# Kernel tuning notes

Hardware: AMD Instinct MI355X
Metric: run time of the kernel (lower is better)

## Reference

```python
import jax, jax.numpy as jnp
import numpy as np

B, N, D = 8, 10000, 16
E = 320000
EH, EOUT, NOUT = 32, 30, 64

def setup_inputs() -> dict:
    key = jax.random.key(0)
    ks = jax.random.split(key, 12)
    x = jax.random.normal(ks[0], (B, N, D), dtype=jnp.float32)
    edge_index = jax.random.randint(ks[1], (2, E), 0, N, dtype=jnp.int32)
    # edge_attr: col 0 = city distance (keep away from 0), col 1 = direction
    dist = jax.random.uniform(ks[2], (E,), dtype=jnp.float32) * 100.0 + 1.0
    direc = jax.random.uniform(ks[3], (E,), dtype=jnp.float32) * 360.0
    edge_attr = jnp.stack([dist, direc], axis=-1)
    wind_mean = jnp.array([3.0, 180.0], dtype=jnp.float32)
    wind_std = jnp.array([1.5, 90.0], dtype=jnp.float32)
    W1 = jax.random.normal(ks[4], (2 * D + 2 + 1, EH), dtype=jnp.float32) * 0.1
    b1 = jnp.zeros((EH,), dtype=jnp.float32)
    W2 = jax.random.normal(ks[5], (EH, EOUT), dtype=jnp.float32) * 0.1
    b2 = jnp.zeros((EOUT,), dtype=jnp.float32)
    Wn = jax.random.normal(ks[6], (EOUT, NOUT), dtype=jnp.float32) * 0.1
    bn = jnp.zeros((NOUT,), dtype=jnp.float32)
    return {"x": x, "edge_index": edge_index, "edge_attr": edge_attr,
            "wind_mean": wind_mean, "wind_std": wind_std,
            "W1": W1, "b1": b1, "W2": W2, "b2": b2, "Wn": Wn, "bn": bn}

def reference(x, edge_index, edge_attr, wind_mean, wind_std, W1, b1, W2, b2, Wn, bn):
    src, tgt = edge_index[0], edge_index[1]
    node_src = x[:, src]      # [B, E, D]
    node_tgt = x[:, tgt]      # [B, E, D]
    # de-normalize wind features (last 2 channels)
    src_wind = node_src[:, :, -2:] * wind_std[None, None, :] + wind_mean[None, None, :]
    speed = src_wind[:, :, 0]
    direc = src_wind[:, :, 1]
    city_dist = edge_attr[:, 0][None, :]   # [1, E]
    city_direc = edge_attr[:, 1][None, :]
    theta = jnp.abs(city_direc - direc)
    edge_weight = jax.nn.relu(3.0 * speed * jnp.cos(theta) / city_dist)  # [B, E]
    # normalized edge attributes (torch std is unbiased)
    ea_norm = (edge_attr - edge_attr.mean(axis=0)) / jnp.std(edge_attr, axis=0, ddof=1)
    ea_norm_b = jnp.broadcast_to(ea_norm[None, :, :], (x.shape[0], ea_norm.shape[0], 2))
    feat = jnp.concatenate([node_src, node_tgt, ea_norm_b, edge_weight[:, :, None]], axis=-1)  # [B, E, 2D+3]
    h = jax.nn.sigmoid(feat @ W1 + b1)
    e = jax.nn.sigmoid(h @ W2 + b2)        # [B, E, EOUT]
    agg = jnp.zeros((x.shape[0], x.shape[1], e.shape[-1]), dtype=e.dtype)
    agg = agg.at[:, tgt].add(e)
    agg = agg.at[:, src].add(-e)
    out = jax.nn.sigmoid(agg @ Wn + bn)    # [B, N, NOUT]
    return out
```

## Files before the change

### kernel.cpp

```cpp
#include <hip/hip_runtime.h>
#include <hip/hip_bf16.h>
#include <math.h>

#define B 8
#define N 10000
#define D 16
#define E 320000
#define EH 32
#define EOUT 30
#define NOUT 64
#define FEAT 35
#define FILL_BLOCKS ((E + 255) / 256)
#define PQ_BLOCKS   ((B * N * 64) / 256)

typedef short bf16x8 __attribute__((ext_vector_type(8)));
typedef float f32x4 __attribute__((ext_vector_type(4)));

#define LDS_FENCE() asm volatile("" ::: "memory")

__device__ __forceinline__ float sigmoidf_(float v) {
    return __builtin_amdgcn_rcpf(1.0f + __expf(-v));
}

__device__ __forceinline__ unsigned int pack_bf16_2(float a, float b) {
    unsigned ua = __float_as_uint(a), ub = __float_as_uint(b);
    ua = (ua + 0x7FFFu + ((ua >> 16) & 1u)) >> 16;
    ub = (ub + 0x7FFFu + ((ub >> 16) & 1u)) >> 16;
    return ua | (ub << 16);
}

__device__ __forceinline__ unsigned short bf16rn(float f) {
    unsigned u = __float_as_uint(f);
    u = (u + 0x7FFFu + ((u >> 16) & 1u)) >> 16;
    return (unsigned short)u;
}

__global__ void stats_count_kernel(const float* __restrict__ ea,
                                   const int* __restrict__ eidx,
                                   float* __restrict__ stats,
                                   int* __restrict__ cnt) {
    float s0 = 0.f, s1 = 0.f, q0 = 0.f, q1 = 0.f;
    for (int i = blockIdx.x * blockDim.x + threadIdx.x; i < E; i += gridDim.x * blockDim.x) {
        float2 v = *(const float2*)(ea + 2 * (size_t)i);
        s0 += v.x; q0 += v.x * v.x;
        s1 += v.y; q1 += v.y * v.y;
        atomicAdd(&cnt[eidx[E + i]], 1);
        atomicAdd(&cnt[N + eidx[i]], 1);
    }
    #pragma unroll
    for (int off = 32; off > 0; off >>= 1) {
        s0 += __shfl_down(s0, off);
        s1 += __shfl_down(s1, off);
        q0 += __shfl_down(q0, off);
        q1 += __shfl_down(q1, off);
    }
    if ((threadIdx.x & 63) == 0) {
        atomicAdd(&stats[0], s0);
        atomicAdd(&stats[1], s1);
        atomicAdd(&stats[2], q0);
        atomicAdd(&stats[3], q1);
    }
}

__global__ void __launch_bounds__(1024) scan_kernel(const int* __restrict__ cnt_in,
                                                    int* __restrict__ offs,
                                                    int* __restrict__ cursor,
                                                    float* __restrict__ stats,
                                                    const float* __restrict__ W2,
                                                    unsigned short* __restrict__ w2f) {
    if (threadIdx.x == 0) {
        const float n = (float)E;
        float s0 = stats[0], s1 = stats[1], q0 = stats[2], q1 = stats[3];
        float v0 = (q0 - s0 * s0 / n) / (n - 1.0f);
        float v1 = (q1 - s1 * s1 / n) / (n - 1.0f);
        stats[4] = s0 / n;
        stats[5] = 1.0f / sqrtf(v0);
        stats[6] = s1 / n;
        stats[7] = 1.0f / sqrtf(v1);
    }
    if (threadIdx.x < 128) {
        int tl = threadIdx.x >> 6;
        int ln = threadIdx.x & 63;
        int k0 = (ln >> 4) * 8;
        int col = tl * 16 + (ln & 15);
        unsigned short* hi = w2f + ((size_t)(tl * 2 + 0) * 64 + ln) * 8;
        unsigned short* lo = w2f + ((size_t)(tl * 2 + 1) * 64 + ln) * 8;
        #pragma unroll
        for (int j = 0; j < 8; j++) {
            float w = (col < EOUT) ? W2[(k0 + j) * EOUT + col] : 0.0f;
            unsigned u = __float_as_uint(w) & 0xFFFF0000u;
            float r = w - __uint_as_float(u);
            hi[j] = (unsigned short)(u >> 16);
            lo[j] = bf16rn(r);
        }
    }
    const int M = 2 * N;
    const int CH = 20;
    __shared__ int lds[1024];
    int t = threadIdx.x;
    int base = t * CH;
    int loc[CH];
    int s = 0;
    #pragma unroll
    for (int i = 0; i < CH; i++) {
        int idx = base + i;
        int v = (idx < M) ? cnt_in[idx] : 0;
        loc[i] = s;
        s += v;
    }
    lds[t] = s;
    __syncthreads();
    for (int off = 1; off < 1024; off <<= 1) {
        int v = (t >= off) ? lds[t - off] : 0;
        __syncthreads();
        lds[t] += v;
        __syncthreads();
    }
    int tbase = (t > 0) ? lds[t - 1] : 0;
    #pragma unroll
    for (int i = 0; i < CH; i++) {
        int idx = base + i;
        if (idx < M) {
            offs[idx] = tbase + loc[i];
            cursor[idx] = tbase + loc[i];
        }
    }
    if (t == 1023) offs[M] = lds[1023];
}

__global__ void __launch_bounds__(256) fill_pq_kernel(
    const int* __restrict__ eidx, int* __restrict__ cursor,
    int* __restrict__ lists,
    const float* __restrict__ x, const float* __restrict__ W1,
    const float* __restrict__ b1,
    unsigned short* __restrict__ Pb, unsigned short* __restrict__ Qb)
{
    if (blockIdx.x < FILL_BLOCKS) {
        int e = blockIdx.x * 256 + threadIdx.x;
        if (e >= E) return;
        int p = atomicAdd(&cursor[eidx[E + e]], 1);
        lists[p] = e;
        int q = atomicAdd(&cursor[N + eidx[e]], 1);
        lists[q] = e;
    } else {
        int wid = ((blockIdx.x - FILL_BLOCKS) * 256 + threadIdx.x) >> 6;
        int lane = threadIdx.x & 63;
        if (wid >= B * N) return;
        int j = lane & 31;
        int half = lane >> 5;
        const float* xr = x + (size_t)wid * D;
        float acc = half ? b1[j] : 0.f;
        const float* Wb = W1 + (half ? D * EH : 0);
        #pragma unroll
        for (int d = 0; d < D; d++)
            acc = fmaf(xr[d], Wb[d * EH + j], acc);
        float accN = __shfl_down(acc, 1);
        if (!(lane & 1)) {
            unsigned u = pack_bf16_2(acc, accN);
            unsigned short* dst = (half ? Qb : Pb) + (size_t)wid * EH + j;
            *(unsigned*)dst = u;
        }
    }
}

__global__ void __launch_bounds__(256) edge_mlp_kernel(
    const float* __restrict__ x, const int* __restrict__ eidx,
    const float* __restrict__ ea,
    const float* __restrict__ wind_mean, const float* __restrict__ wind_std,
    const float* __restrict__ W1, const float* __restrict__ b2,
    const float* __restrict__ stats,
    const unsigned short* __restrict__ Pb, const unsigned short* __restrict__ Qb,
    const unsigned short* __restrict__ w2f,
    unsigned short* __restrict__ eBuf, int b0, int nb)
{
    __shared__ unsigned short hsh[4][64][64];

    int t = blockIdx.x * blockDim.x + threadIdx.x;
    if (t >= nb * E) return;
    int bb = t / E;
    int e = t - bb * E;
    int b = b0 + bb;
    int wv = threadIdx.x >> 6;
    int lane = threadIdx.x & 63;

    int src = eidx[e];
    int tgt = eidx[E + e];

    const uint4* Pr = (const uint4*)(Pb + ((size_t)b * N + src) * EH);
    const uint4* Qr = (const uint4*)(Qb + ((size_t)b * N + tgt) * EH);

    float h[EH];
    #pragma unroll
    for (int i = 0; i < 4; i++) {
        uint4 p = Pr[i];
        uint4 q = Qr[i];
        unsigned pu[4] = {p.x, p.y, p.z, p.w};
        unsigned qu[4] = {q.x, q.y, q.z, q.w};
        #pragma unroll
        for (int k2 = 0; k2 < 4; k2++) {
            float pl = __uint_as_float(pu[k2] << 16);
            float ph = __uint_as_float(pu[k2] & 0xFFFF0000u);
            float ql = __uint_as_float(qu[k2] << 16);
            float qh = __uint_as_float(qu[k2] & 0xFFFF0000u);
            h[8 * i + 2 * k2 + 0] = pl + ql;
            h[8 * i + 2 * k2 + 1] = ph + qh;
        }
    }

    float2 eav = *(const float2*)(ea + 2 * (size_t)e);
    float dist = eav.x, cdir = eav.y;
    float f32v = (dist - stats[4]) * stats[5];
    float f33v = (cdir - stats[6]) * stats[7];

    float2 xw = *(const float2*)(x + ((size_t)b * N + src) * D + 14);
    float speed = xw.x * wind_std[0] + wind_mean[0];
    float sdir  = xw.y * wind_std[1] + wind_mean[1];
    float ew = fmaxf(3.0f * speed * __cosf(fabsf(cdir - sdir)) *
                     __builtin_amdgcn_rcpf(dist), 0.0f);

    const float* W1r32 = W1 + 32 * EH;
    const float* W1r33 = W1 + 33 * EH;
    const float* W1r34 = W1 + 34 * EH;
    #pragma unroll
    for (int j = 0; j < EH; j++) {
        float v = h[j];
        v = fmaf(f32v, W1r32[j], v);
        v = fmaf(f33v, W1r33[j], v);
        v = fmaf(ew,   W1r34[j], v);
        h[j] = sigmoidf_(v);
    }

    unsigned short* myrow = &hsh[wv][lane][0];
    int lx = lane & 7;
    #pragma unroll
    for (int i = 0; i < 4; i++) {
        unsigned hw[4], lw[4];
        #pragma unroll
        for (int p = 0; p < 4; p++) {
            float f0 = h[8 * i + 2 * p];
            float f1 = h[8 * i + 2 * p + 1];
            unsigned u0 = __float_as_uint(f0) & 0xFFFF0000u;
            unsigned u1 = __float_as_uint(f1) & 0xFFFF0000u;
            float r0 = f0 - __uint_as_float(u0);
            float r1 = f1 - __uint_as_float(u1);
            hw[p] = (u0 >> 16) | u1;
            lw[p] = pack_bf16_2(r0, r1);
        }
        *(uint4*)(myrow + ((i ^ lx) << 3))       = make_uint4(hw[0], hw[1], hw[2], hw[3]);
        *(uint4*)(myrow + (((4 + i) ^ lx) << 3)) = make_uint4(lw[0], lw[1], lw[2], lw[3]);
    }
    LDS_FENCE();

    union { uint4 u; bf16x8 v; } bf[4];
    const uint4* wfp = (const uint4*)w2f;
    #pragma unroll
    for (int i = 0; i < 4; i++) bf[i].u = wfp[i * 64 + lane];

    int m  = lane & 15;
    int hr = lane >> 4;
    float bias0 = b2[m];
    float bias1 = (m < EOUT - 16) ? b2[16 + m] : 0.0f;

    f32x4 acc[4][2];
    #pragma unroll
    for (int g = 0; g < 4; g++) {
        f32x4 z0 = {bias0, bias0, bias0, bias0};
        f32x4 z1 = {bias1, bias1, bias1, bias1};
        acc[g][0] = z0;
        acc[g][1] = z1;
    }

    int mx = m & 7;
    #pragma unroll
    for (int g = 0; g < 4; g++) {
        const unsigned short* rp = &hsh[wv][g * 16 + m][0];
        bf16x8 Ah = *(const bf16x8*)(rp + ((hr ^ mx) << 3));
        bf16x8 Al = *(const bf16x8*)(rp + (((4 + hr) ^ mx) << 3));
        acc[g][0] = __builtin_amdgcn_mfma_f32_16x16x32_bf16(Ah, bf[0].v, acc[g][0], 0, 0, 0);
        acc[g][1] = __builtin_amdgcn_mfma_f32_16x16x32_bf16(Ah, bf[2].v, acc[g][1], 0, 0, 0);
        acc[g][0] = __builtin_amdgcn_mfma_f32_16x16x32_bf16(Al, bf[0].v, acc[g][0], 0, 0, 0);
        acc[g][1] = __builtin_amdgcn_mfma_f32_16x16x32_bf16(Al, bf[2].v, acc[g][1], 0, 0, 0);
        acc[g][0] = __builtin_amdgcn_mfma_f32_16x16x32_bf16(Ah, bf[1].v, acc[g][0], 0, 0, 0);
        acc[g][1] = __builtin_amdgcn_mfma_f32_16x16x32_bf16(Ah, bf[3].v, acc[g][1], 0, 0, 0);
    }
    LDS_FENCE();

    unsigned short* wb = &hsh[wv][0][0];
    int c0 = m >> 3;
    int c1 = 2 + (m >> 3);
    int mp = m & 7;
    #pragma unroll
    for (int g = 0; g < 4; g++) {
        #pragma unroll
        for (int j = 0; j < 4; j++) {
            int er  = g * 16 + hr * 4 + j;
            int swz = ((hr & 1) << 2) | j;
            float v0 = sigmoidf_(acc[g][0][j]);
            float v1 = sigmoidf_(acc[g][1][j]);
            wb[er * 64 + ((c0 ^ swz) << 3) + mp] = bf16rn(v0);
            wb[er * 64 + ((c1 ^ swz) << 3) + mp] =
                (m < 14) ? bf16rn(v1) : (unsigned short)0;
        }
    }
    LDS_FENCE();

    int eWaveBase = e - lane;
    int rrow = lane >> 2;
    int rx   = rrow & 7;
    unsigned short* wdst = eBuf + ((size_t)bb * E + eWaveBase) * EH;
    #pragma unroll
    for (int i = 0; i < 4; i++) {
        uint4 v = *(const uint4*)(wb + (i * 16 + rrow) * 64 + (((lane & 3) ^ rx) << 3));
        *(uint4*)(wdst + i * 512 + lane * 8) = v;
    }
}

__global__ void __launch_bounds__(256) gather_kernel(
    const unsigned short* __restrict__ eBuf, const int* __restrict__ offs,
    const int* __restrict__ lists, const float* __restrict__ Wn,
    const float* __restrict__ bn, float* __restrict__ out, int b0, int nb)
{
    int wid = (blockIdx.x * blockDim.x + threadIdx.x) >> 6;
    int lane = threadIdx.x & 63;
    if (wid >= nb * N) return;
    int bb = wid / N;
    int node = wid - bb * N;
    int b = b0 + bb;

    int g = lane >> 2;
    int c = lane & 3;
    const uint4* ebase = (const uint4*)(eBuf + (size_t)bb * E * EH);

    float a0 = 0.f, a1 = 0.f, a2 = 0.f, a3 = 0.f;
    float a4 = 0.f, a5 = 0.f, a6 = 0.f, a7 = 0.f;

    {
        int s = offs[node], e1 = offs[node + 1];
        for (int r = s; r < e1; r += 16) {
            int row = r + g;
            if (row < e1) {
                int eid = lists[row];
                uint4 v = ebase[(size_t)eid * 4 + c];
                a0 += __uint_as_float(v.x << 16);
                a1 += __uint_as_float(v.x & 0xFFFF0000u);
                a2 += __uint_as_float(v.y << 16);
                a3 += __uint_as_float(v.y & 0xFFFF0000u);
                a4 += __uint_as_float(v.z << 16);
                a5 += __uint_as_float(v.z & 0xFFFF0000u);
                a6 += __uint_as_float(v.w << 16);
                a7 += __uint_as_float(v.w & 0xFFFF0000u);
            }
        }
    }
    {
        int s = offs[N + node], e1 = offs[N + node + 1];
        for (int r = s; r < e1; r += 16) {
            int row = r + g;
            if (row < e1) {
                int eid = lists[row];
                uint4 v = ebase[(size_t)eid * 4 + c];
                a0 -= __uint_as_float(v.x << 16);
                a1 -= __uint_as_float(v.x & 0xFFFF0000u);
                a2 -= __uint_as_float(v.y << 16);
                a3 -= __uint_as_float(v.y & 0xFFFF0000u);
                a4 -= __uint_as_float(v.z << 16);
                a5 -= __uint_as_float(v.z & 0xFFFF0000u);
                a6 -= __uint_as_float(v.w << 16);
                a7 -= __uint_as_float(v.w & 0xFFFF0000u);
            }
        }
    }

    #pragma unroll
    for (int off = 4; off <= 32; off <<= 1) {
        a0 += __shfl_xor(a0, off); a1 += __shfl_xor(a1, off);
        a2 += __shfl_xor(a2, off); a3 += __shfl_xor(a3, off);
        a4 += __shfl_xor(a4, off); a5 += __shfl_xor(a5, off);
        a6 += __shfl_xor(a6, off); a7 += __shfl_xor(a7, off);
    }

    float o = bn[lane];
    #pragma unroll
    for (int k = 0; k < EOUT; k++) {
        float av;
        switch (k & 7) {
            case 0:  av = a0; break;
            case 1:  av = a1; break;
            case 2:  av = a2; break;
            case 3:  av = a3; break;
            case 4:  av = a4; break;
            case 5:  av = a5; break;
            case 6:  av = a6; break;
            default: av = a7; break;
        }
        float ak = __shfl(av, k >> 3);
        o = fmaf(ak, Wn[k * NOUT + lane], o);
    }
    out[((size_t)b * N + node) * NOUT + lane] = sigmoidf_(o);
}

__global__ void __launch_bounds__(256) edge_kernel_atomic(
    const float* __restrict__ x, const int* __restrict__ eidx,
    const float* __restrict__ ea,
    const float* __restrict__ wind_mean, const float* __restrict__ wind_std,
    const float* __restrict__ W1, const float* __restrict__ b1,
    const float* __restrict__ W2, const float* __restrict__ b2,
    const float* __restrict__ stats, float* __restrict__ agg)
{
    int t = blockIdx.x * blockDim.x + threadIdx.x;
    if (t >= B * E) return;
    int b = t / E;
    int e = t - b * E;
    int src = eidx[e];
    int tgt = eidx[E + e];
    const float* xs = x + ((size_t)b * N + src) * D;
    const float* xt = x + ((size_t)b * N + tgt) * D;
    float f[FEAT];
    #pragma unroll
    for (int i = 0; i < D; i++) f[i] = xs[i];
    #pragma unroll
    for (int i = 0; i < D; i++) f[D + i] = xt[i];
    float2 eav = *(const float2*)(ea + 2 * (size_t)e);
    f[32] = (eav.x - stats[4]) * stats[5];
    f[33] = (eav.y - stats[6]) * stats[7];
    float speed = f[14] * wind_std[0] + wind_mean[0];
    float sdir  = f[15] * wind_std[1] + wind_mean[1];
    f[34] = fmaxf(3.0f * speed * cosf(fabsf(eav.y - sdir)) / eav.x, 0.0f);
    float h[EH];
    #pragma unroll
    for (int j = 0; j < EH; j++) h[j] = b1[j];
    #pragma unroll
    for (int k = 0; k < FEAT; k++) {
        float fk = f[k];
        #pragma unroll
        for (int j = 0; j < EH; j++) h[j] = fmaf(fk, W1[k * EH + j], h[j]);
    }
    #pragma unroll
    for (int j = 0; j < EH; j++) h[j] = sigmoidf_(h[j]);
    float o[EOUT];
    #pragma unroll
    for (int j = 0; j < EOUT; j++) o[j] = b2[j];
    #pragma unroll
    for (int k = 0; k < EH; k++) {
        float hk = h[k];
        #pragma unroll
        for (int j = 0; j < EOUT; j++) o[j] = fmaf(hk, W2[k * EOUT + j], o[j]);
    }
    float* at = agg + ((size_t)b * N + tgt) * EOUT;
    float* as = agg + ((size_t)b * N + src) * EOUT;
    #pragma unroll
    for (int j = 0; j < EOUT; j++) {
        float v = sigmoidf_(o[j]);
        atomicAdd(at + j,  v);
        atomicAdd(as + j, -v);
    }
}

__global__ void __launch_bounds__(256) node_kernel_fallback(
    const float* __restrict__ agg, const float* __restrict__ Wn,
    const float* __restrict__ bn, float* __restrict__ out)
{
    int t = blockIdx.x * blockDim.x + threadIdx.x;
    if (t >= B * N * NOUT) return;
    int row = t >> 6;
    int j   = t & 63;
    const float* a = agg + (size_t)row * EOUT;
    float acc = bn[j];
    #pragma unroll
    for (int k = 0; k < EOUT; k++) acc = fmaf(a[k], Wn[k * NOUT + j], acc);
    out[t] = sigmoidf_(acc);
}

extern "C" void kernel_launch(void* const* d_in, const int* in_sizes, int n_in,
                              void* d_out, int out_size, void* d_ws, size_t ws_size,
                              hipStream_t stream) {
    const float* x         = (const float*)d_in[0];
    const int*   eidx      = (const int*)d_in[1];
    const float* ea        = (const float*)d_in[2];
    const float* wind_mean = (const float*)d_in[3];
    const float* wind_std  = (const float*)d_in[4];
    const float* W1        = (const float*)d_in[5];
    const float* b1        = (const float*)d_in[6];
    const float* W2        = (const float*)d_in[7];
    const float* b2        = (const float*)d_in[8];
    const float* Wn        = (const float*)d_in[9];
    const float* bn        = (const float*)d_in[10];
    float* out = (float*)d_out;

    char* ws = (char*)d_ws;
    float*          stats = (float*)(ws + 0);
    unsigned short* w2f   = (unsigned short*)(ws + 256);
    int*            offs  = (int*)(ws + 4352);
    int*            cnt   = (int*)(ws + 84480);
    int*            lists = (int*)(ws + 164608);
    unsigned short* Pb    = (unsigned short*)(ws + 2724608);
    unsigned short* Qb    = (unsigned short*)(ws + 7844608);
    unsigned short* eBuf  = (unsigned short*)(ws + 12964608);
    const size_t fixed = 12964608;
    const size_t perBatch = (size_t)E * EH * sizeof(unsigned short);

    if (ws_size >= fixed + perBatch) {
        int chunk = (int)((ws_size - fixed) / perBatch);
        if (chunk > 8) chunk = 8;

        hipMemsetAsync(ws, 0, 164608, stream);

        stats_count_kernel<<<256, 256, 0, stream>>>(ea, eidx, stats, cnt);
        scan_kernel<<<1, 1024, 0, stream>>>(cnt, offs, cnt, stats, W2, w2f);
        fill_pq_kernel<<<FILL_BLOCKS + PQ_BLOCKS, 256, 0, stream>>>(
            eidx, cnt, lists, x, W1, b1, Pb, Qb);

        for (int b0 = 0; b0 < B; b0 += chunk) {
            int nb = B - b0; if (nb > chunk) nb = chunk;
            int nwork = nb * E;
            edge_mlp_kernel<<<(nwork + 255) / 256, 256, 0, stream>>>(
                x, eidx, ea, wind_mean, wind_std, W1, b2, stats,
                Pb, Qb, w2f, eBuf, b0, nb);
            gather_kernel<<<nb * (N * 64 / 256), 256, 0, stream>>>(
                eBuf, offs, lists, Wn, bn, out, b0, nb);
        }
    } else {
        float* agg = (float*)(ws + 164608);
        size_t zero_bytes = 164608 + (size_t)B * N * EOUT * sizeof(float);
        hipMemsetAsync(ws, 0, zero_bytes, stream);
        stats_count_kernel<<<256, 256, 0, stream>>>(ea, eidx, stats, cnt);
        scan_kernel<<<1, 1024, 0, stream>>>(cnt, offs, cnt, stats, W2, w2f);
        int nwork = B * E;
        edge_kernel_atomic<<<(nwork + 255) / 256, 256, 0, stream>>>(
            x, eidx, ea, wind_mean, wind_std, W1, b1, W2, b2, stats, agg);
        int nout_elems = B * N * NOUT;
        node_kernel_fallback<<<(nout_elems + 255) / 256, 256, 0, stream>>>(
            agg, Wn, bn, out);
    }
}
```

Measured before the change: 401.1 us.

## Merge stats with P/Q precompute, fold list fill into edge MLP, drop split-bf16

Combines the stats/count pass with the per-node P/Q projection into one launch. Moves the CSR list fill into extra blocks of the first edge-MLP launch, removing a separate kernel. Also drops the hi/lo bf16 split of the hidden activations, so the second layer uses a single bf16 operand and two fewer MFMAs per group. Using plain bf16 lowers the accuracy of the hidden layer. The edge-block count is now computed as nb*E/256 with no tail guard, which relies on E being a multiple of 256.

```diff
diff --git a/kernel.cpp b/kernel.cpp
--- a/kernel.cpp
+++ b/kernel.cpp
@@ -33,6 +33,56 @@
     unsigned u = __float_as_uint(f);
     u = (u + 0x7FFFu + ((u >> 16) & 1u)) >> 16;
     return (unsigned short)u;
+}
+
+__global__ void __launch_bounds__(256) stats_pq_kernel(
+    const float* __restrict__ ea, const int* __restrict__ eidx,
+    float* __restrict__ stats, int* __restrict__ cnt,
+    const float* __restrict__ x, const float* __restrict__ W1,
+    const float* __restrict__ b1,
+    unsigned short* __restrict__ Pb, unsigned short* __restrict__ Qb)
+{
+    if (blockIdx.x < 256) {
+        float s0 = 0.f, s1 = 0.f, q0 = 0.f, q1 = 0.f;
+        for (int i = blockIdx.x * 256 + threadIdx.x; i < E; i += 256 * 256) {
+            float2 v = *(const float2*)(ea + 2 * (size_t)i);
+            s0 += v.x; q0 += v.x * v.x;
+            s1 += v.y; q1 += v.y * v.y;
+            atomicAdd(&cnt[eidx[E + i]], 1);
+            atomicAdd(&cnt[N + eidx[i]], 1);
+        }
+        #pragma unroll
+        for (int off = 32; off > 0; off >>= 1) {
+            s0 += __shfl_down(s0, off);
+            s1 += __shfl_down(s1, off);
+            q0 += __shfl_down(q0, off);
+            q1 += __shfl_down(q1, off);
+        }
+        if ((threadIdx.x & 63) == 0) {
+            atomicAdd(&stats[0], s0);
+            atomicAdd(&stats[1], s1);
+            atomicAdd(&stats[2], q0);
+            atomicAdd(&stats[3], q1);
+        }
+    } else {
+        int wid = ((blockIdx.x - 256) * 256 + threadIdx.x) >> 6;
+        int lane = threadIdx.x & 63;
+        if (wid >= B * N) return;
+        int j = lane & 31;
+        int half = lane >> 5;
+        const float* xr = x + (size_t)wid * D;
+        float acc = half ? b1[j] : 0.f;
+        const float* Wb = W1 + (half ? D * EH : 0);
+        #pragma unroll
+        for (int d = 0; d < D; d++)
+            acc = fmaf(xr[d], Wb[d * EH + j], acc);
+        float accN = __shfl_down(acc, 1);
+        if (!(lane & 1)) {
+            unsigned u = pack_bf16_2(acc, accN);
+            unsigned short* dst = (half ? Qb : Pb) + (size_t)wid * EH + j;
+            *(unsigned*)dst = u;
+        }
+    }
 }
 
 __global__ void stats_count_kernel(const float* __restrict__ ea,
@@ -128,41 +178,6 @@
     if (t == 1023) offs[M] = lds[1023];
 }
 
-__global__ void __launch_bounds__(256) fill_pq_kernel(
-    const int* __restrict__ eidx, int* __restrict__ cursor,
-    int* __restrict__ lists,
-    const float* __restrict__ x, const float* __restrict__ W1,
-    const float* __restrict__ b1,
-    unsigned short* __restrict__ Pb, unsigned short* __restrict__ Qb)
-{
-    if (blockIdx.x < FILL_BLOCKS) {
-        int e = blockIdx.x * 256 + threadIdx.x;
-        if (e >= E) return;
-        int p = atomicAdd(&cursor[eidx[E + e]], 1);
-        lists[p] = e;
-        int q = atomicAdd(&cursor[N + eidx[e]], 1);
-        lists[q] = e;
-    } else {
-        int wid = ((blockIdx.x - FILL_BLOCKS) * 256 + threadIdx.x) >> 6;
-        int lane = threadIdx.x & 63;
-        if (wid >= B * N) return;
-        int j = lane & 31;
-        int half = lane >> 5;
-        const float* xr = x + (size_t)wid * D;
-        float acc = half ? b1[j] : 0.f;
-        const float* Wb = W1 + (half ? D * EH : 0);
-        #pragma unroll
-        for (int d = 0; d < D; d++)
-            acc = fmaf(xr[d], Wb[d * EH + j], acc);
-        float accN = __shfl_down(acc, 1);
-        if (!(lane & 1)) {
-            unsigned u = pack_bf16_2(acc, accN);
-            unsigned short* dst = (half ? Qb : Pb) + (size_t)wid * EH + j;
-            *(unsigned*)dst = u;
-        }
-    }
-}
-
 __global__ void __launch_bounds__(256) edge_mlp_kernel(
     const float* __restrict__ x, const int* __restrict__ eidx,
     const float* __restrict__ ea,
@@ -171,12 +186,24 @@
     const float* __restrict__ stats,
     const unsigned short* __restrict__ Pb, const unsigned short* __restrict__ Qb,
     const unsigned short* __restrict__ w2f,
-    unsigned short* __restrict__ eBuf, int b0, int nb)
+    unsigned short* __restrict__ eBuf,
+    int* __restrict__ cursor, int* __restrict__ lists,
+    int b0, int eblk)
 {
     __shared__ unsigned short hsh[4][64][64];
 
-    int t = blockIdx.x * blockDim.x + threadIdx.x;
-    if (t >= nb * E) return;
+    if ((int)blockIdx.x >= eblk) {
+        int e = (blockIdx.x - eblk) * 256 + threadIdx.x;
+        if (e < E) {
+            int p = atomicAdd(&cursor[eidx[E + e]], 1);
+            lists[p] = e;
+            int q = atomicAdd(&cursor[N + eidx[e]], 1);
+            lists[q] = e;
+        }
+        return;
+    }
+
+    int t = blockIdx.x * 256 + threadIdx.x;
     int bb = t / E;
     int e = t - bb * E;
     int b = b0 + bb;
@@ -234,20 +261,11 @@
     int lx = lane & 7;
     #pragma unroll
     for (int i = 0; i < 4; i++) {
-        unsigned hw[4], lw[4];
-        #pragma unroll
-        for (int p = 0; p < 4; p++) {
-            float f0 = h[8 * i + 2 * p];
-            float f1 = h[8 * i + 2 * p + 1];
-            unsigned u0 = __float_as_uint(f0) & 0xFFFF0000u;
-            unsigned u1 = __float_as_uint(f1) & 0xFFFF0000u;
-            float r0 = f0 - __uint_as_float(u0);
-            float r1 = f1 - __uint_as_float(u1);
-            hw[p] = (u0 >> 16) | u1;
-            lw[p] = pack_bf16_2(r0, r1);
-        }
-        *(uint4*)(myrow + ((i ^ lx) << 3))       = make_uint4(hw[0], hw[1], hw[2], hw[3]);
-        *(uint4*)(myrow + (((4 + i) ^ lx) << 3)) = make_uint4(lw[0], lw[1], lw[2], lw[3]);
+        unsigned hw[4];
+        #pragma unroll
+        for (int p = 0; p < 4; p++)
+            hw[p] = pack_bf16_2(h[8 * i + 2 * p], h[8 * i + 2 * p + 1]);
+        *(uint4*)(myrow + ((i ^ lx) << 3)) = make_uint4(hw[0], hw[1], hw[2], hw[3]);
     }
     LDS_FENCE();
 
@@ -275,11 +293,8 @@
     for (int g = 0; g < 4; g++) {
         const unsigned short* rp = &hsh[wv][g * 16 + m][0];
         bf16x8 Ah = *(const bf16x8*)(rp + ((hr ^ mx) << 3));
-        bf16x8 Al = *(const bf16x8*)(rp + (((4 + hr) ^ mx) << 3));
         acc[g][0] = __builtin_amdgcn_mfma_f32_16x16x32_bf16(Ah, bf[0].v, acc[g][0], 0, 0, 0);
         acc[g][1] = __builtin_amdgcn_mfma_f32_16x16x32_bf16(Ah, bf[2].v, acc[g][1], 0, 0, 0);
-        acc[g][0] = __builtin_amdgcn_mfma_f32_16x16x32_bf16(Al, bf[0].v, acc[g][0], 0, 0, 0);
-        acc[g][1] = __builtin_amdgcn_mfma_f32_16x16x32_bf16(Al, bf[2].v, acc[g][1], 0, 0, 0);
         acc[g][0] = __builtin_amdgcn_mfma_f32_16x16x32_bf16(Ah, bf[1].v, acc[g][0], 0, 0, 0);
         acc[g][1] = __builtin_amdgcn_mfma_f32_16x16x32_bf16(Ah, bf[3].v, acc[g][1], 0, 0, 0);
     }
@@ -505,17 +520,17 @@
 
         hipMemsetAsync(ws, 0, 164608, stream);
 
-        stats_count_kernel<<<256, 256, 0, stream>>>(ea, eidx, stats, cnt);
+        stats_pq_kernel<<<256 + PQ_BLOCKS, 256, 0, stream>>>(
+            ea, eidx, stats, cnt, x, W1, b1, Pb, Qb);
         scan_kernel<<<1, 1024, 0, stream>>>(cnt, offs, cnt, stats, W2, w2f);
-        fill_pq_kernel<<<FILL_BLOCKS + PQ_BLOCKS, 256, 0, stream>>>(
-            eidx, cnt, lists, x, W1, b1, Pb, Qb);
 
         for (int b0 = 0; b0 < B; b0 += chunk) {
             int nb = B - b0; if (nb > chunk) nb = chunk;
-            int nwork = nb * E;
-            edge_mlp_kernel<<<(nwork + 255) / 256, 256, 0, stream>>>(
+            int eblk = nb * E / 256;
+            int grid = eblk + ((b0 == 0) ? FILL_BLOCKS : 0);
+            edge_mlp_kernel<<<grid, 256, 0, stream>>>(
                 x, eidx, ea, wind_mean, wind_std, W1, b2, stats,
-                Pb, Qb, w2f, eBuf, b0, nb);
+                Pb, Qb, w2f, eBuf, cnt, lists, b0, eblk);
             gather_kernel<<<nb * (N * 64 / 256), 256, 0, stream>>>(
                 eBuf, offs, lists, Wn, bn, out, b0, nb);
         }
```

Measured after the change: 388.8 us. 3.1% less time.
